# Performance work log

Hardware: AMD Instinct MI355X
Metric: run time of the kernel (lower is better)

The kernel has to match this reference:

```python
import jax, jax.numpy as jnp
import numpy as np

B, CIN, COUT, K, NS, NIN, H = 4, 128, 128, 9, 16384, 16384, 64
W0 = 30.0  # SIREN first-layer frequency


def setup_inputs() -> dict:
    ks = jax.random.split(jax.random.key(0), 8)
    x = jax.random.normal(ks[0], (B, CIN, NIN), dtype=jnp.float32)
    neighbours = jax.random.randint(ks[1], (K, NS), 0, NIN)
    # normalized relative neighbour coordinates in [-1, 1], shape (K*NS, 2)
    coords = 2.0 * jax.random.uniform(ks[2], (K * NS, 2), dtype=jnp.float32) - 1.0
    W1 = jax.random.normal(ks[3], (2, H), dtype=jnp.float32) / jnp.sqrt(2.0)
    b1 = jnp.zeros((H,), dtype=jnp.float32)
    W2 = jax.random.normal(ks[4], (H, H), dtype=jnp.float32) / jnp.sqrt(H * 1.0)
    b2 = jnp.zeros((H,), dtype=jnp.float32)
    W3 = jax.random.normal(ks[5], (H, COUT * CIN), dtype=jnp.float32) / jnp.sqrt(H * 1.0)
    b3 = jnp.zeros((COUT * CIN,), dtype=jnp.float32)
    bias = jnp.zeros((1, COUT, 1), dtype=jnp.float32)
    return {"x": x, "neighbours": neighbours, "coords": coords,
            "W1": W1, "b1": b1, "W2": W2, "b2": b2, "W3": W3, "b3": b3,
            "bias": bias}


def reference(x, neighbours, coords, W1, b1, W2, b2, W3, b3, bias):
    k, ns = neighbours.shape
    cin = x.shape[1]
    cout = W3.shape[1] // cin
    # INR filter generation: (K*NS, 2) -> (K*NS, COUT*CIN)
    h = jnp.sin(W0 * (coords @ W1 + b1))
    h = jnp.sin(h @ W2 + b2)
    f = h @ W3 + b3                                  # (K*NS, COUT*CIN)
    # (K*NS, COUT, CIN) -> (COUT, CIN, K, NS), matching torch permute(1,2,0).reshape
    f = f.reshape(k * ns, cout, cin).transpose(1, 2, 0).reshape(cout, cin, k, ns)
    # neighbor gather: (B, CIN, K, NS)
    x_unfold = x[:, :, neighbours]
    # weighted reduce over (CIN, K) per output location
    out = jnp.einsum('bjkl,ijkl->bil', x_unfold, f)
    return out + bias
```

## Files before the change

kernel.cpp:

```cpp
#include <hip/hip_runtime.h>

#define NS   16384
#define NIN  16384
#define CIN  128
#define COUT 128
#define KNB  9
#define MCH  66
#define QDIM (CIN*MCH)
#define W0C  30.0f

typedef __bf16 bf16;
typedef bf16  bf16x8  __attribute__((ext_vector_type(8)));
typedef bf16  bf16x2  __attribute__((ext_vector_type(2)));
typedef unsigned short u16;
typedef u16   u16x8   __attribute__((ext_vector_type(8)));
typedef float floatx4 __attribute__((ext_vector_type(4)));
typedef unsigned int u32;

__device__ inline u16 f2bf(float f){
  u32 u = __float_as_uint(f);
  u += 0x7fffu + ((u >> 16) & 1u);
  return (u16)(u >> 16);
}
__device__ inline float bf2f(u16 s){
  return __uint_as_float((u32)s << 16);
}
__device__ inline u32 cvtpk2(float lo, float hi){
  u32 r; asm("v_cvt_pk_bf16_f32 %0, %1, %2" : "=v"(r) : "v"(lo), "v"(hi)); return r;
}

#if defined(__has_builtin)
# if __has_builtin(__builtin_amdgcn_fdot2_f32_bf16)
#  define HAVE_DOT2 1
# endif
#endif
#ifndef HAVE_DOT2
# define HAVE_DOT2 0
#endif

__device__ inline float dot2bf(u32 x2, u32 h2, float c){
#if HAVE_DOT2
  return __builtin_amdgcn_fdot2_f32_bf16(__builtin_bit_cast(bf16x2, x2),
                                         __builtin_bit_cast(bf16x2, h2), c, false);
#else
  float xl = bf2f((u16)(x2 & 0xffffu)), xh = bf2f((u16)(x2 >> 16));
  float hl = bf2f((u16)(h2 & 0xffffu)), hh = bf2f((u16)(h2 >> 16));
  return fmaf(xh, hh, fmaf(xl, hl, c));
#endif
}

#define WG_BARRIER() do { \
  asm volatile("s_waitcnt lgkmcnt(0)" ::: "memory"); \
  __builtin_amdgcn_s_barrier(); \
} while (0)

__global__ void k0_vt(const float* __restrict__ W3, const float* __restrict__ b3,
                      u16* __restrict__ Vt){
  int idx = blockIdx.x*256 + threadIdx.x;
  if (idx >= COUT*QDIM) return;
  int i = idx / QDIM;
  int q = idx - i*QDIM;
  int m = q >> 7;
  int j = q & 127;
  float v = 0.f;
  if (m < 64)       v = W3[m*16384 + i*128 + j];
  else if (m == 64) v = b3[i*128 + j];
  Vt[idx] = f2bf(v);
}

__global__ __launch_bounds__(256) void k1_mlp(const float* __restrict__ coords,
      const float* __restrict__ W1, const float* __restrict__ b1,
      const float* __restrict__ W2, const float* __restrict__ b2,
      u16* __restrict__ h){
  int lane = threadIdx.x & 63;
  int pt = blockIdx.x*4 + (threadIdx.x >> 6);
  float c0 = coords[2*pt], c1 = coords[2*pt+1];
  float z  = fmaf(c0, W1[lane], fmaf(c1, W1[64+lane], b1[lane]));
  float h1 = sinf(W0C * z);
  float acc = b2[lane];
  #pragma unroll
  for (int mp = 0; mp < 64; ++mp)
    acc = fmaf(__shfl(h1, mp, 64), W2[mp*64 + lane], acc);
  float h2 = sinf(acc);
  size_t base = (size_t)pt * MCH;
  h[base + lane] = f2bf(h2);
  if (lane == 0){ h[base+64] = 0x3F80; h[base+65] = 0; }
}

__global__ __launch_bounds__(256) void k1kp(const u16* __restrict__ h,
                                            u32* __restrict__ hK){
  __shared__ u16 t[KNB][32][66];
  int l0 = blockIdx.x*32;
  int tid = threadIdx.x;
  for (int e = tid; e < KNB*32*66; e += 256){
    int k = e / (32*66);
    int r = e - k*32*66;
    int l = r / 66;
    int m = r - l*66;
    t[k][l][m] = h[((size_t)(k<<14) + l0 + l)*MCH + m];
  }
  __syncthreads();
  for (int e = tid; e < 66*5*32; e += 256){
    int m  = e / 160;
    int r  = e - m*160;
    int kp = r >> 5;
    int l  = r & 31;
    u32 lo = t[2*kp][l][m];
    u32 hi = (kp < 4) ? (u32)t[2*kp+1][l][m] : 0u;
    hK[(((size_t)m*5 + kp) << 14) + l0 + l] = lo | (hi << 16);
  }
}

__global__ void k_tr(const float* __restrict__ x, u16* __restrict__ xT){
  __shared__ __align__(16) float t[32][33];
  int b  = blockIdx.z;
  int j0 = blockIdx.y*32;
  int p0 = blockIdx.x*32;
  int tx = threadIdx.x, ty = threadIdx.y;
  const float* xb  = x  + (size_t)b*CIN*NIN;
  u16*         xTb = xT + (size_t)b*NIN*CIN;
  #pragma unroll
  for (int n = 0; n < 4; ++n)
    t[ty+8*n][tx] = xb[(size_t)(j0+ty+8*n)*NIN + p0+tx];
  __syncthreads();
  #pragma unroll
  for (int n = 0; n < 4; ++n)
    xTb[(size_t)(p0+ty+8*n)*CIN + j0+tx] = f2bf(t[tx][ty+8*n]);
}

__global__ __launch_bounds__(512, 4) void k_fused(
      const u16* __restrict__ xT,
      const u32* __restrict__ hK,
      const int* __restrict__ nb,
      const u16* __restrict__ Vt,
      const float* __restrict__ bias,
      float* __restrict__ out){
  __shared__ __align__(16) u16 A[2][2][32][136];
  __shared__ u32 hs[2][2][5][32];
  __shared__ int pk[KNB][32];

  const int tid = threadIdx.x;
  const int r0  = blockIdx.x * 32;
  const int b   = r0 >> 14;
  const int l0  = r0 & (NS-1);

  if (tid < KNB*32){
    int k = tid >> 5, l = tid & 31;
    pk[k][l] = nb[k*NS + l0 + l];
  }
  WG_BARRIER();

  const int lq = tid >> 4;
  const int jc = tid & 15;

  const bool hact = tid < 320;
  const int  hs_  = tid / 160;
  const int  hr_  = tid - hs_*160;
  const int  hkp_ = hr_ >> 5;
  const int  hl_  = hr_ & 31;
  const u32* hKp  = hK + (((size_t)(5*hs_ + hkp_)) << 14) + l0 + hl_;
  const size_t HSTR = (size_t)10 << 14;
  u32 hra = 0, hrb = 0;
  if (hact){
    u32 h0 = hKp[0];
    hra = hKp[HSTR];
    hrb = hKp[2*HSTR];
    hs[0][hs_][hkp_][hl_] = h0;
  }

  const char* xbB = (const char*)(xT + ((size_t)b << 21));
  u32 xp[5][8];
  #pragma unroll
  for (int kp = 0; kp < 4; ++kp){
    u16x8 ga = *(const u16x8*)(xbB + (((size_t)(u32)pk[2*kp  ][lq]) << 8) + (size_t)jc*16);
    u16x8 gb = *(const u16x8*)(xbB + (((size_t)(u32)pk[2*kp+1][lq]) << 8) + (size_t)jc*16);
    #pragma unroll
    for (int j = 0; j < 8; ++j) xp[kp][j] = (u32)ga[j] | ((u32)gb[j] << 16);
  }
  {
    u16x8 ga = *(const u16x8*)(xbB + (((size_t)(u32)pk[8][lq]) << 8) + (size_t)jc*16);
    #pragma unroll
    for (int j = 0; j < 8; ++j) xp[4][j] = (u32)ga[j];
  }

  const int lane  = tid & 63;
  const int w     = tid >> 6;
  const int ar    = lane & 15;
  const int klane = lane >> 4;

  floatx4 acc[2];
  acc[0] = (floatx4){0.f,0.f,0.f,0.f};
  acc[1] = (floatx4){0.f,0.f,0.f,0.f};

  const char* VtB = (const char*)Vt + (size_t)(w*16 + ar)*(QDIM*2) + (size_t)klane*16;

  bf16x8 bv[8];
  #pragma unroll
  for (int mm = 0; mm < 2; ++mm)
    #pragma unroll
    for (int kt = 0; kt < 4; ++kt)
      bv[mm*4+kt] = *(const bf16x8*)(VtB + mm*256 + kt*64);

  WG_BARRIER();

  for (int mg = 0; mg < 33; ++mg){
    const int pb = mg & 1;

    float a2[2][8];
    #pragma unroll
    for (int s = 0; s < 2; ++s)
      #pragma unroll
      for (int j = 0; j < 8; ++j) a2[s][j] = 0.f;
    #pragma unroll
    for (int s = 0; s < 2; ++s){
      #pragma unroll
      for (int kp = 0; kp < 5; ++kp){
        u32 hp = hs[pb][s][kp][lq];
        #pragma unroll
        for (int j = 0; j < 8; ++j)
          a2[s][j] = dot2bf(xp[kp][j], hp, a2[s][j]);
      }
    }
    {
      uint4 q0, q1;
      q0.x = cvtpk2(a2[0][0], a2[0][1]); q0.y = cvtpk2(a2[0][2], a2[0][3]);
      q0.z = cvtpk2(a2[0][4], a2[0][5]); q0.w = cvtpk2(a2[0][6], a2[0][7]);
      q1.x = cvtpk2(a2[1][0], a2[1][1]); q1.y = cvtpk2(a2[1][2], a2[1][3]);
      q1.z = cvtpk2(a2[1][4], a2[1][5]); q1.w = cvtpk2(a2[1][6], a2[1][7]);
      *(uint4*)&A[pb][0][lq][jc*8] = q0;
      *(uint4*)&A[pb][1][lq][jc*8] = q1;
    }

    if (hact){
      if (mg < 32) hs[pb^1][hs_][hkp_][hl_] = hra;
      hra = hrb;
      if (mg <= 29) hrb = hKp[(size_t)(mg+3)*HSTR];
    }

    WG_BARRIER();

    #pragma unroll
    for (int mm = 0; mm < 2; ++mm){
      const char* Ab = (const char*)&A[pb][mm][0][0] + (size_t)klane*16;
      #pragma unroll
      for (int kt = 0; kt < 4; ++kt){
        bf16x8 av0 = *(const bf16x8*)(Ab + (     ar)*272 + kt*64);
        bf16x8 av1 = *(const bf16x8*)(Ab + (16 + ar)*272 + kt*64);
        acc[0] = __builtin_amdgcn_mfma_f32_16x16x32_bf16(av0, bv[mm*4+kt], acc[0], 0, 0, 0);
        acc[1] = __builtin_amdgcn_mfma_f32_16x16x32_bf16(av1, bv[mm*4+kt], acc[1], 0, 0, 0);
      }
    }

    if (mg < 32){
      const char* Vg = VtB + (size_t)(mg+1)*512;
      #pragma unroll
      for (int mm = 0; mm < 2; ++mm)
        #pragma unroll
        for (int kt = 0; kt < 4; ++kt)
          bv[mm*4+kt] = *(const bf16x8*)(Vg + mm*256 + kt*64);
    }
  }

  float* ob = out + ((size_t)b << 21);
  int i = w*16 + ar;
  float bi = bias[i];
  #pragma unroll
  for (int rf = 0; rf < 2; ++rf){
    int l = l0 + rf*16 + klane*4;
    float4 v;
    v.x = acc[rf][0] + bi;
    v.y = acc[rf][1] + bi;
    v.z = acc[rf][2] + bi;
    v.w = acc[rf][3] + bi;
    *(float4*)(ob + ((size_t)i << 14) + l) = v;
  }
}

__global__ __launch_bounds__(256) void k_naive(const float* __restrict__ x,
      const int* __restrict__ nb, const float* __restrict__ coords,
      const float* __restrict__ W1, const float* __restrict__ b1,
      const float* __restrict__ W2, const float* __restrict__ b2,
      const float* __restrict__ W3, const float* __restrict__ b3,
      const float* __restrict__ bias, float* __restrict__ out){
  __shared__ __align__(16) float hk[KNB][68];
  __shared__ int pk[KNB];
  __shared__ __align__(16) float xg[4][KNB][128];
  __shared__ __align__(16) float ul[128][66];
  int tid = threadIdx.x;
  int l = blockIdx.x;
  int lane = tid & 63, wid = tid >> 6;
  if (tid < KNB) pk[tid] = nb[tid*NS + l];
  for (int k = wid; k < KNB; k += 4){
    int pt = k*NS + l;
    float c0 = coords[2*pt], c1 = coords[2*pt+1];
    float z  = fmaf(c0, W1[lane], fmaf(c1, W1[64+lane], b1[lane]));
    float h1 = sinf(W0C*z);
    float a = b2[lane];
    for (int mp = 0; mp < 64; ++mp)
      a = fmaf(__shfl(h1, mp, 64), W2[mp*64+lane], a);
    hk[k][lane] = sinf(a);
    if (lane == 0){ hk[k][64] = 1.f; hk[k][65] = 0.f; }
  }
  __syncthreads();
  for (int idx = tid; idx < 4*KNB*128; idx += 256){
    int b = idx / (KNB*128);
    int r = idx - b*KNB*128;
    int k = r >> 7;
    int j = r & 127;
    xg[b][k][j] = x[((size_t)b*CIN + j)*NIN + pk[k]];
  }
  __syncthreads();
  for (int b = 0; b < 4; ++b){
    for (int idx = tid; idx < 128*65; idx += 256){
      int j = idx / 65, m = idx - j*65;
      float s = 0.f;
      for (int k = 0; k < KNB; ++k) s = fmaf(xg[b][k][j], hk[k][m], s);
      ul[j][m] = s;
    }
    __syncthreads();
    if (tid < 128){
      int i = tid;
      float v = bias[i];
      for (int j = 0; j < 128; ++j){
        const float* wcol = W3 + i*128 + j;
        for (int m = 0; m < 64; ++m)
          v = fmaf(ul[j][m], wcol[(size_t)m*16384], v);
        v = fmaf(ul[j][64], b3[i*128+j], v);
      }
      out[((size_t)b<<21) + ((size_t)i<<14) + l] = v;
    }
    __syncthreads();
  }
}

extern "C" void kernel_launch(void* const* d_in, const int* in_sizes, int n_in,
                              void* d_out, int out_size, void* d_ws, size_t ws_size,
                              hipStream_t stream) {
  const float* x      = (const float*)d_in[0];
  const int*   nb     = (const int*)  d_in[1];
  const float* coords = (const float*)d_in[2];
  const float* W1     = (const float*)d_in[3];
  const float* b1     = (const float*)d_in[4];
  const float* W2     = (const float*)d_in[5];
  const float* b2     = (const float*)d_in[6];
  const float* W3     = (const float*)d_in[7];
  const float* b3     = (const float*)d_in[8];
  const float* bias   = (const float*)d_in[9];
  float* out = (float*)d_out;

  const size_t VT_BYTES = (size_t)COUT*QDIM*2;
  const size_t HK_BYTES = (size_t)MCH*5*NS*4;
  const size_t H_BYTES  = (size_t)KNB*NS*MCH*2;
  const size_t FIXED    = VT_BYTES + HK_BYTES + H_BYTES;

  if (ws_size >= FIXED) {
    char* ws = (char*)d_ws;
    unsigned short* Vt = (unsigned short*)ws;
    u32*            hK = (u32*)(ws + VT_BYTES);
    unsigned short* h  = (unsigned short*)(ws + VT_BYTES + HK_BYTES);
    unsigned short* xT = h;

    k0_vt<<<(COUT*QDIM + 255)/256, 256, 0, stream>>>(W3, b3, Vt);
    k1_mlp<<<(KNB*NS)/4, 256, 0, stream>>>(coords, W1, b1, W2, b2, h);
    k1kp<<<NS/32, 256, 0, stream>>>(h, hK);
    k_tr<<<dim3(NIN/32, CIN/32, 4), dim3(32, 8), 0, stream>>>(x, xT);
    k_fused<<<(4*NS)/32, 512, 0, stream>>>(xT, hK, nb, Vt, bias, out);
  } else {
    k_naive<<<NS, 256, 0, stream>>>(x, nb, coords, W1, b1, W2, b2, W3, b3, bias, out);
  }
  (void)in_sizes; (void)n_in; (void)out_size;
}
```

Before: 691.6 us.

## Retile fused kernel to cover all batches per block sharing hK tiles

The fused kernel now gives each 1024-thread block 16 output locations across all 4 batches instead of 32 locations of one batch. The neighbour indices and hK coefficient tiles are loaded once and shared by the four batches, which cuts redundant hK traffic. Each wave now owns 32 output channels for one batch and reads the V weights straight from global memory inside the MFMA loop instead of prefetching them into registers. That removes the register-prefetch overlap and raises per-iteration global/L2 load pressure, and __launch_bounds__(1024,4) may force register limits or spills.

After: 1.256 ms. 1.82x slower.

```diff
diff --git a/kernel.cpp b/kernel.cpp
--- a/kernel.cpp
+++ b/kernel.cpp
@@ -128,47 +128,46 @@
     xTb[(size_t)(p0+ty+8*n)*CIN + j0+tx] = f2bf(t[tx][ty+8*n]);
 }
 
-__global__ __launch_bounds__(512, 4) void k_fused(
+__global__ __launch_bounds__(1024, 4) void k_fused(
       const u16* __restrict__ xT,
       const u32* __restrict__ hK,
       const int* __restrict__ nb,
       const u16* __restrict__ Vt,
       const float* __restrict__ bias,
       float* __restrict__ out){
-  __shared__ __align__(16) u16 A[2][2][32][136];
-  __shared__ u32 hs[2][2][5][32];
-  __shared__ int pk[KNB][32];
+  __shared__ __align__(16) u16 A[2][4][2][16][136];
+  __shared__ u32 hs[2][2][5][16];
+  __shared__ int pk[KNB][16];
 
   const int tid = threadIdx.x;
-  const int r0  = blockIdx.x * 32;
-  const int b   = r0 >> 14;
-  const int l0  = r0 & (NS-1);
-
-  if (tid < KNB*32){
-    int k = tid >> 5, l = tid & 31;
+  const int l0  = blockIdx.x * 16;
+
+  if (tid < KNB*16){
+    int k = tid >> 4, l = tid & 15;
     pk[k][l] = nb[k*NS + l0 + l];
   }
   WG_BARRIER();
 
-  const int lq = tid >> 4;
+  const int bb = tid >> 8;
+  const int lq = (tid >> 4) & 15;
   const int jc = tid & 15;
 
-  const bool hact = tid < 320;
-  const int  hs_  = tid / 160;
-  const int  hr_  = tid - hs_*160;
-  const int  hkp_ = hr_ >> 5;
-  const int  hl_  = hr_ & 31;
-  const u32* hKp  = hK + (((size_t)(5*hs_ + hkp_)) << 14) + l0 + hl_;
+  const bool hact = tid < 160;
+  const int  hss  = tid / 80;
+  const int  hrr  = tid - hss*80;
+  const int  hkp  = hrr >> 4;
+  const int  hl   = hrr & 15;
+  const u32* hKp  = hK + (((size_t)(5*hss + hkp)) << 14) + l0 + hl;
   const size_t HSTR = (size_t)10 << 14;
   u32 hra = 0, hrb = 0;
   if (hact){
     u32 h0 = hKp[0];
     hra = hKp[HSTR];
     hrb = hKp[2*HSTR];
-    hs[0][hs_][hkp_][hl_] = h0;
-  }
-
-  const char* xbB = (const char*)(xT + ((size_t)b << 21));
+    hs[0][hss][hkp][hl] = h0;
+  }
+
+  const char* xbB = (const char*)(xT + ((size_t)bb << 21));
   u32 xp[5][8];
   #pragma unroll
   for (int kp = 0; kp < 4; ++kp){
@@ -185,6 +184,8 @@
 
   const int lane  = tid & 63;
   const int w     = tid >> 6;
+  const int bw    = w >> 2;
+  const int iq    = w & 3;
   const int ar    = lane & 15;
   const int klane = lane >> 4;
 
@@ -192,14 +193,8 @@
   acc[0] = (floatx4){0.f,0.f,0.f,0.f};
   acc[1] = (floatx4){0.f,0.f,0.f,0.f};
 
-  const char* VtB = (const char*)Vt + (size_t)(w*16 + ar)*(QDIM*2) + (size_t)klane*16;
-
-  bf16x8 bv[8];
-  #pragma unroll
-  for (int mm = 0; mm < 2; ++mm)
-    #pragma unroll
-    for (int kt = 0; kt < 4; ++kt)
-      bv[mm*4+kt] = *(const bf16x8*)(VtB + mm*256 + kt*64);
+  const char* VtB0 = (const char*)Vt + (size_t)(iq*32      + ar)*(QDIM*2) + (size_t)klane*16;
+  const char* VtB1 = (const char*)Vt + (size_t)(iq*32 + 16 + ar)*(QDIM*2) + (size_t)klane*16;
 
   WG_BARRIER();
 
@@ -227,51 +222,46 @@
       q0.z = cvtpk2(a2[0][4], a2[0][5]); q0.w = cvtpk2(a2[0][6], a2[0][7]);
       q1.x = cvtpk2(a2[1][0], a2[1][1]); q1.y = cvtpk2(a2[1][2], a2[1][3]);
       q1.z = cvtpk2(a2[1][4], a2[1][5]); q1.w = cvtpk2(a2[1][6], a2[1][7]);
-      *(uint4*)&A[pb][0][lq][jc*8] = q0;
-      *(uint4*)&A[pb][1][lq][jc*8] = q1;
+      *(uint4*)&A[pb][bb][0][lq][jc*8] = q0;
+      *(uint4*)&A[pb][bb][1][lq][jc*8] = q1;
     }
 
     if (hact){
-      if (mg < 32) hs[pb^1][hs_][hkp_][hl_] = hra;
+      if (mg < 32) hs[pb^1][hss][hkp][hl] = hra;
       hra = hrb;
       if (mg <= 29) hrb = hKp[(size_t)(mg+3)*HSTR];
     }
 
     WG_BARRIER();
 
+    const size_t vgofs = (size_t)(mg*2)*256;
     #pragma unroll
     for (int mm = 0; mm < 2; ++mm){
-      const char* Ab = (const char*)&A[pb][mm][0][0] + (size_t)klane*16;
+      const char* Ab = (const char*)&A[pb][bw][mm][0][0] + (size_t)klane*16;
+      const char* Vg0 = VtB0 + vgofs + mm*256;
+      const char* Vg1 = VtB1 + vgofs + mm*256;
       #pragma unroll
       for (int kt = 0; kt < 4; ++kt){
-        bf16x8 av0 = *(const bf16x8*)(Ab + (     ar)*272 + kt*64);
-        bf16x8 av1 = *(const bf16x8*)(Ab + (16 + ar)*272 + kt*64);
-        acc[0] = __builtin_amdgcn_mfma_f32_16x16x32_bf16(av0, bv[mm*4+kt], acc[0], 0, 0, 0);
-        acc[1] = __builtin_amdgcn_mfma_f32_16x16x32_bf16(av1, bv[mm*4+kt], acc[1], 0, 0, 0);
+        bf16x8 av  = *(const bf16x8*)(Ab + ar*272 + kt*64);
+        bf16x8 bv0 = *(const bf16x8*)(Vg0 + kt*64);
+        bf16x8 bv1 = *(const bf16x8*)(Vg1 + kt*64);
+        acc[0] = __builtin_amdgcn_mfma_f32_16x16x32_bf16(av, bv0, acc[0], 0, 0, 0);
+        acc[1] = __builtin_amdgcn_mfma_f32_16x16x32_bf16(av, bv1, acc[1], 0, 0, 0);
       }
     }
-
-    if (mg < 32){
-      const char* Vg = VtB + (size_t)(mg+1)*512;
-      #pragma unroll
-      for (int mm = 0; mm < 2; ++mm)
-        #pragma unroll
-        for (int kt = 0; kt < 4; ++kt)
-          bv[mm*4+kt] = *(const bf16x8*)(Vg + mm*256 + kt*64);
-    }
-  }
-
-  float* ob = out + ((size_t)b << 21);
-  int i = w*16 + ar;
-  float bi = bias[i];
-  #pragma unroll
-  for (int rf = 0; rf < 2; ++rf){
-    int l = l0 + rf*16 + klane*4;
+  }
+
+  float* ob = out + ((size_t)bw << 21);
+  #pragma unroll
+  for (int cf = 0; cf < 2; ++cf){
+    int i = iq*32 + cf*16 + ar;
+    float bi = bias[i];
+    int l = l0 + klane*4;
     float4 v;
-    v.x = acc[rf][0] + bi;
-    v.y = acc[rf][1] + bi;
-    v.z = acc[rf][2] + bi;
-    v.w = acc[rf][3] + bi;
+    v.x = acc[cf][0] + bi;
+    v.y = acc[cf][1] + bi;
+    v.z = acc[cf][2] + bi;
+    v.w = acc[cf][3] + bi;
     *(float4*)(ob + ((size_t)i << 14) + l) = v;
   }
 }
@@ -364,7 +354,7 @@
     k1_mlp<<<(KNB*NS)/4, 256, 0, stream>>>(coords, W1, b1, W2, b2, h);
     k1kp<<<NS/32, 256, 0, stream>>>(h, hK);
     k_tr<<<dim3(NIN/32, CIN/32, 4), dim3(32, 8), 0, stream>>>(x, xT);
-    k_fused<<<(4*NS)/32, 512, 0, stream>>>(xT, hK, nb, Vt, bias, out);
+    k_fused<<<NS/16, 1024, 0, stream>>>(xT, hK, nb, Vt, bias, out);
   } else {
     k_naive<<<NS, 256, 0, stream>>>(x, nb, coords, W1, b1, W2, b2, W3, b3, bias, out);
   }
```

## Split K across wave halves with 2x2 MFMA tiles and LDS reduction

Applied to the files above, without the earlier changes.

Waves are regrouped into four output-channel groups of 32 and two K halves. Each wave now computes a 2x2 block of 16x16 MFMA tiles over half of the K range, so every A fragment read from LDS feeds two MFMAs instead of one, halving LDS reads per MFMA. The two K halves are combined at the end through an LDS reduction that reuses the A buffer, before bias is added and the result stored. This adds one extra barrier pair and more live accumulator registers, which could affect occupancy.

Result: no change. 691.0 us (-0.1%).

```diff
diff --git a/kernel.cpp b/kernel.cpp
--- a/kernel.cpp
+++ b/kernel.cpp
@@ -185,21 +185,29 @@
 
   const int lane  = tid & 63;
   const int w     = tid >> 6;
+  const int iq    = w & 3;
+  const int kh    = w >> 2;
   const int ar    = lane & 15;
   const int klane = lane >> 4;
 
-  floatx4 acc[2];
-  acc[0] = (floatx4){0.f,0.f,0.f,0.f};
-  acc[1] = (floatx4){0.f,0.f,0.f,0.f};
-
-  const char* VtB = (const char*)Vt + (size_t)(w*16 + ar)*(QDIM*2) + (size_t)klane*16;
-
-  bf16x8 bv[8];
+  floatx4 acc[2][2];
+  #pragma unroll
+  for (int r = 0; r < 2; ++r)
+    #pragma unroll
+    for (int f = 0; f < 2; ++f)
+      acc[r][f] = (floatx4){0.f,0.f,0.f,0.f};
+
+  const char* VtB0 = (const char*)Vt + (size_t)(iq*32      + ar)*(QDIM*2) + (size_t)(kh*128 + klane*16);
+  const char* VtB1 = (const char*)Vt + (size_t)(iq*32 + 16 + ar)*(QDIM*2) + (size_t)(kh*128 + klane*16);
+
+  bf16x8 bv[2][4];
   #pragma unroll
   for (int mm = 0; mm < 2; ++mm)
     #pragma unroll
-    for (int kt = 0; kt < 4; ++kt)
-      bv[mm*4+kt] = *(const bf16x8*)(VtB + mm*256 + kt*64);
+    for (int kt = 0; kt < 2; ++kt){
+      bv[0][mm*2+kt] = *(const bf16x8*)(VtB0 + mm*256 + kt*64);
+      bv[1][mm*2+kt] = *(const bf16x8*)(VtB1 + mm*256 + kt*64);
+    }
 
   WG_BARRIER();
 
@@ -241,38 +249,58 @@
 
     #pragma unroll
     for (int mm = 0; mm < 2; ++mm){
-      const char* Ab = (const char*)&A[pb][mm][0][0] + (size_t)klane*16;
+      const char* Ab = (const char*)&A[pb][mm][0][0] + kh*128 + klane*16;
       #pragma unroll
-      for (int kt = 0; kt < 4; ++kt){
+      for (int kt = 0; kt < 2; ++kt){
         bf16x8 av0 = *(const bf16x8*)(Ab + (     ar)*272 + kt*64);
         bf16x8 av1 = *(const bf16x8*)(Ab + (16 + ar)*272 + kt*64);
-        acc[0] = __builtin_amdgcn_mfma_f32_16x16x32_bf16(av0, bv[mm*4+kt], acc[0], 0, 0, 0);
-        acc[1] = __builtin_amdgcn_mfma_f32_16x16x32_bf16(av1, bv[mm*4+kt], acc[1], 0, 0, 0);
+        acc[0][0] = __builtin_amdgcn_mfma_f32_16x16x32_bf16(av0, bv[0][mm*2+kt], acc[0][0], 0, 0, 0);
+        acc[0][1] = __builtin_amdgcn_mfma_f32_16x16x32_bf16(av0, bv[1][mm*2+kt], acc[0][1], 0, 0, 0);
+        acc[1][0] = __builtin_amdgcn_mfma_f32_16x16x32_bf16(av1, bv[0][mm*2+kt], acc[1][0], 0, 0, 0);
+        acc[1][1] = __builtin_amdgcn_mfma_f32_16x16x32_bf16(av1, bv[1][mm*2+kt], acc[1][1], 0, 0, 0);
       }
     }
 
     if (mg < 32){
-      const char* Vg = VtB + (size_t)(mg+1)*512;
+      const char* Vg0 = VtB0 + (size_t)(mg+1)*512;
+      const char* Vg1 = VtB1 + (size_t)(mg+1)*512;
       #pragma unroll
       for (int mm = 0; mm < 2; ++mm)
         #pragma unroll
-        for (int kt = 0; kt < 4; ++kt)
-          bv[mm*4+kt] = *(const bf16x8*)(Vg + mm*256 + kt*64);
-    }
-  }
-
-  float* ob = out + ((size_t)b << 21);
-  int i = w*16 + ar;
-  float bi = bias[i];
-  #pragma unroll
-  for (int rf = 0; rf < 2; ++rf){
-    int l = l0 + rf*16 + klane*4;
-    float4 v;
-    v.x = acc[rf][0] + bi;
-    v.y = acc[rf][1] + bi;
-    v.z = acc[rf][2] + bi;
-    v.w = acc[rf][3] + bi;
-    *(float4*)(ob + ((size_t)i << 14) + l) = v;
+        for (int kt = 0; kt < 2; ++kt){
+          bv[0][mm*2+kt] = *(const bf16x8*)(Vg0 + mm*256 + kt*64);
+          bv[1][mm*2+kt] = *(const bf16x8*)(Vg1 + mm*256 + kt*64);
+        }
+    }
+  }
+
+  WG_BARRIER();
+  floatx4* red = (floatx4*)&A[0][0][0][0];
+  if (kh == 1){
+    floatx4* dst = red + (((size_t)iq*64 + lane) << 2);
+    dst[0] = acc[0][0]; dst[1] = acc[0][1]; dst[2] = acc[1][0]; dst[3] = acc[1][1];
+  }
+  WG_BARRIER();
+  if (kh == 0){
+    const floatx4* src = red + (((size_t)iq*64 + lane) << 2);
+    acc[0][0] += src[0]; acc[0][1] += src[1];
+    acc[1][0] += src[2]; acc[1][1] += src[3];
+    float* ob = out + ((size_t)b << 21);
+    #pragma unroll
+    for (int rf = 0; rf < 2; ++rf){
+      #pragma unroll
+      for (int f = 0; f < 2; ++f){
+        int i = iq*32 + f*16 + ar;
+        float bi = bias[i];
+        int l = l0 + rf*16 + klane*4;
+        float4 v;
+        v.x = acc[rf][f][0] + bi;
+        v.y = acc[rf][f][1] + bi;
+        v.z = acc[rf][f][2] + bi;
+        v.w = acc[rf][f][3] + bi;
+        *(float4*)(ob + ((size_t)i << 14) + l) = v;
+      }
+    }
   }
 }
 
```
